# Kernel tuning notes

Hardware: AMD Instinct MI355X
Metric: run time of the kernel (lower is better)

The kernel has to match this reference:

```python
import jax, jax.numpy as jnp
import numpy as np

B, F, S, P, E, H = 64, 32, 512, 96, 8, 2048
TOP_K = 2
ALPHA = 10.0
ENT_EPS = 1e-8
CV_EPS = 1e-10


def setup_inputs() -> dict:
    key = jax.random.key(0)
    ks = jax.random.split(key, 8)
    s = 0.02
    return {
        "x": jax.random.normal(ks[0], (B, F, S), dtype=jnp.float32),
        "time_embedding": jax.random.normal(ks[1], (B, F, S), dtype=jnp.float32),
        "Wg": jax.random.normal(ks[2], (S, E), dtype=jnp.float32) * s,
        "bg": jnp.zeros((E,), dtype=jnp.float32),
        "W1": jax.random.normal(ks[3], (E, S, H), dtype=jnp.float32) * s,
        "b1": jnp.zeros((E, H), dtype=jnp.float32),
        "W2": jax.random.normal(ks[4], (E, H, P), dtype=jnp.float32) * s,
        "b2": jnp.zeros((E, P), dtype=jnp.float32),
    }


def _gates(tf, Wg, bg):
    # tf: [F, B, S] -> logits [F, B, E]
    logits = jnp.einsum('fbs,se->fbe', tf, Wg) + bg
    # kthvalue(x, E - top_k + 1) = (E - top_k)-th entry (0-based) of ascending sort = k-th largest
    kth = jnp.sort(logits, axis=-1)[..., E - TOP_K]  # [F, B]
    mask = logits < kth[..., None]
    sm = jax.nn.softmax(logits, axis=-1)
    dec = jnp.where(mask, ALPHA * jnp.log(sm + 1.0), ALPHA * (jnp.exp(sm) - 1.0))
    return jax.nn.softmax(dec, axis=-1)  # [F, B, E]


def reference(x, time_embedding, Wg, bg, W1, b1, W2, b2):
    xf = jnp.transpose(x, (1, 0, 2))               # [F, B, S]
    tf = jnp.transpose(time_embedding, (1, 0, 2))  # [F, B, S]
    gates = _gates(tf, Wg, bg)                     # [F, B, E]

    # all experts on all features (eval mode: dropout = identity)
    h = jax.nn.gelu(jnp.einsum('fbs,esh->febh', xf, W1) + b1[None, :, None, :], approximate=False)
    eo = jnp.einsum('febh,ehp->febp', h, W2) + b2[None, :, None, :]  # [F, E, B, P]
    out = jnp.einsum('fbe,febp->fbp', gates, eo)   # gated weighted sum
    output = jnp.transpose(out, (1, 0, 2))         # [B, F, P]

    # selector loss: cv_squared of importance = gates.sum(batch) expanded over pred_len
    gsum = gates.sum(axis=1)                       # [F, E]
    imp = jnp.broadcast_to(gsum[..., None], (F, E, P)).reshape(F, E * P)
    cv = jnp.var(imp, axis=1, ddof=1) / (jnp.mean(imp, axis=1) ** 2 + CV_EPS)
    selector_loss = jnp.sum(cv)                    # loss_coef = 1.0

    # entropy loss: importance1 = gates.mean(batch) expanded over pred_len
    gmean = gates.mean(axis=1)                     # [F, E]
    imp1 = jnp.broadcast_to(gmean[..., None], (F, E, P))
    entropy_loss = jnp.sum((-imp1 * jnp.log(imp1 + ENT_EPS)).mean(axis=(1, 2)))

    return output, selector_loss, entropy_loss
```

## Files before the change

### kernel.cpp

```cpp
#include <hip/hip_runtime.h>
#include <math.h>

#define B_ 64
#define F_ 32
#define S_ 512
#define P_ 96
#define E_ 8
#define H_ 2048
#define M_ 2048

#define BM 128
#define BH 128
#define BK 64
#define ZSPLIT 2
#define HPZ (H_ / ZSPLIT)
#define NHT (HPZ / BH)
#define NKC (S_ / BK)

typedef __bf16 bf16x8 __attribute__((ext_vector_type(8)));
typedef __bf16 bf16x4 __attribute__((ext_vector_type(4)));
typedef float f32x4 __attribute__((ext_vector_type(4)));

#define MFMA16(a, b, c) __builtin_amdgcn_mfma_f32_16x16x32_bf16((a), (b), (c), 0, 0, 0)

#define GLL16(gp, lp) __builtin_amdgcn_global_load_lds(                     \
    (const __attribute__((address_space(1))) void*)(gp),                    \
    (__attribute__((address_space(3))) void*)(lp), 16, 0, 0)

#define PW4 asm volatile("s_waitcnt vmcnt(4) lgkmcnt(0)\n\ts_barrier" ::: "memory")
#define PW2 asm volatile("s_waitcnt vmcnt(2) lgkmcnt(0)\n\ts_barrier" ::: "memory")
#define PW0 asm volatile("s_waitcnt vmcnt(0) lgkmcnt(0)\n\ts_barrier" ::: "memory")

__device__ __forceinline__ float fast_gelu(float x) {
  float e = __builtin_amdgcn_exp2f(-2.45546696f * x);
  return x * __builtin_amdgcn_rcpf(1.0f + e);
}

#define PREP_GRID 3776

__global__ __launch_bounds__(256) void k_prep(const float* __restrict__ x,
                                              const float* __restrict__ te,
                                              const float* __restrict__ Wg,
                                              const float* __restrict__ bg,
                                              const float* __restrict__ W1,
                                              const float* __restrict__ W2,
                                              __bf16* __restrict__ xbf,
                                              __bf16* __restrict__ w1t,
                                              __bf16* __restrict__ w2t,
                                              float* __restrict__ gates,
                                              float* __restrict__ out) {
  __shared__ float tile[64 * 65];
  const int blk = blockIdx.x;
  const int tid = threadIdx.x;

  if (blk < 2048) {
    int e = blk >> 8, tt = blk & 255;
    int si = tt >> 5, hi = tt & 31;
    const float* src = W1 + (size_t)e * S_ * H_ + (size_t)(si * 64) * H_ + hi * 64;
    {
      int row = tid >> 2;
      int cb = (tid & 3) * 16;
#pragma unroll
      for (int k = 0; k < 4; ++k) {
        f32x4 v = *(const f32x4*)(src + (size_t)row * H_ + cb + k * 4);
#pragma unroll
        for (int u = 0; u < 4; ++u) tile[row * 65 + cb + k * 4 + u] = v[u];
      }
    }
    __syncthreads();
    {
      int h = tid >> 2;
      int sb = (tid & 3) * 16;
      __bf16* dst = w1t + (size_t)e * H_ * S_ + (size_t)(hi * 64 + h) * S_ + si * 64 + sb;
      bf16x8 o0, o1;
#pragma unroll
      for (int k = 0; k < 8; ++k) o0[k] = (__bf16)tile[(sb + k) * 65 + h];
#pragma unroll
      for (int k = 0; k < 8; ++k) o1[k] = (__bf16)tile[(sb + 8 + k) * 65 + h];
      *(bf16x8*)dst = o0;
      *(bf16x8*)(dst + 8) = o1;
    }
    return;
  }
  if (blk < 2560) {
    int t = blk - 2048;
    int e = t >> 6, hi = (t >> 1) & 31, ph = t & 1;
    const float* src = W2 + (size_t)e * H_ * P_ + (size_t)(hi * 64) * P_ + ph * 48;
    {
      int h = tid & 63;
      int seg = tid >> 6;
#pragma unroll
      for (int k = 0; k < 3; ++k) {
        f32x4 v = *(const f32x4*)(src + (size_t)h * P_ + seg * 12 + k * 4);
#pragma unroll
        for (int u = 0; u < 4; ++u) tile[h * 49 + seg * 12 + k * 4 + u] = v[u];
      }
    }
    __syncthreads();
    if (tid < 192) {
      int p = tid >> 2;
      int hb = (tid & 3) * 16;
      __bf16* dst = w2t + (size_t)e * P_ * H_ + (size_t)(ph * 48 + p) * H_ + hi * 64 + hb;
      bf16x8 o0, o1;
#pragma unroll
      for (int k = 0; k < 8; ++k) o0[k] = (__bf16)tile[(hb + k) * 49 + p];
#pragma unroll
      for (int k = 0; k < 8; ++k) o1[k] = (__bf16)tile[(hb + 8 + k) * 49 + p];
      *(bf16x8*)dst = o0;
      *(bf16x8*)(dst + 8) = o1;
    }
    return;
  }
  if (blk < 3072) {
    size_t i = (size_t)(blk - 2560) * 2048 + (size_t)tid * 8;
#pragma unroll
    for (int k = 0; k < 2; ++k) {
      f32x4 v = *(const f32x4*)(x + i + k * 4);
      bf16x4 o = {(__bf16)v[0], (__bf16)v[1], (__bf16)v[2], (__bf16)v[3]};
      *(bf16x4*)(xbf + i + k * 4) = o;
    }
    return;
  }
  if (blk < 3584) {
    int wave = tid >> 6, lane = tid & 63;
    int m = (blk - 3072) * 4 + wave;
    const float* trow = te + (size_t)m * S_;
    float acc[E_];
#pragma unroll
    for (int e = 0; e < E_; ++e) acc[e] = 0.f;
    for (int s = lane; s < S_; s += 64) {
      float t = trow[s];
      const f32x4* wgr = (const f32x4*)(Wg + s * E_);
      f32x4 a = wgr[0], b = wgr[1];
      acc[0] += t * a[0]; acc[1] += t * a[1]; acc[2] += t * a[2]; acc[3] += t * a[3];
      acc[4] += t * b[0]; acc[5] += t * b[1]; acc[6] += t * b[2]; acc[7] += t * b[3];
    }
#pragma unroll
    for (int e = 0; e < E_; ++e) {
#pragma unroll
      for (int off = 32; off > 0; off >>= 1) acc[e] += __shfl_xor(acc[e], off, 64);
    }
    if (lane == 0) {
      float lg[E_];
      float m1 = -3.4e38f, m2 = -3.4e38f;
#pragma unroll
      for (int e = 0; e < E_; ++e) {
        float v = acc[e] + bg[e];
        lg[e] = v;
        if (v > m1) { m2 = m1; m1 = v; }
        else if (v > m2) { m2 = v; }
      }
      float den = 0.f, sm[E_];
#pragma unroll
      for (int e = 0; e < E_; ++e) { sm[e] = expf(lg[e] - m1); den += sm[e]; }
      float inv = 1.f / den;
      float dmax = -3.4e38f, dec[E_];
#pragma unroll
      for (int e = 0; e < E_; ++e) {
        float p = sm[e] * inv;
        float d = (lg[e] < m2) ? (10.f * logf(p + 1.f)) : (10.f * (expf(p) - 1.f));
        dec[e] = d;
        dmax = fmaxf(dmax, d);
      }
      float dden = 0.f;
#pragma unroll
      for (int e = 0; e < E_; ++e) { dec[e] = expf(dec[e] - dmax); dden += dec[e]; }
      float dinv = 1.f / dden;
#pragma unroll
      for (int e = 0; e < E_; ++e) gates[m * E_ + e] = dec[e] * dinv;
    }
    return;
  }
  {
    size_t i = (size_t)(blk - 3584) * 1024 + (size_t)tid * 4;
    f32x4 z4 = {0.f, 0.f, 0.f, 0.f};
    *(f32x4*)(out + i) = z4;
  }
}

__global__ __launch_bounds__(512, 2) void k_experts(
    const __bf16* __restrict__ xbf,
    const __bf16* __restrict__ w1t,
    const __bf16* __restrict__ w2t,
    const float* __restrict__ b1,
    const float* __restrict__ b2,
    const float* __restrict__ gates,
    float* __restrict__ out)
{
  __shared__ __align__(16) __bf16 W1s[4][BH * BK];
  __shared__ __align__(16) __bf16 Xs[3][BM * BK];
  __shared__ __align__(16) __bf16 Hs[BM * 128];

  const int tid = threadIdx.x;

  if (blockIdx.z == ZSPLIT) {
    if (blockIdx.x != 0 || blockIdx.y != 0) return;
    float* gsum = (float*)&W1s[0][0];
    float* cvs  = gsum + F_ * E_;
    float* ents = cvs + F_;
    if (tid < 256) {
      int f = tid >> 3, ee = tid & 7;
      float s = 0.f;
      for (int b = 0; b < B_; ++b) s += gates[(size_t)(b * F_ + f) * E_ + ee];
      gsum[f * E_ + ee] = s;
    }
    __syncthreads();
    if (tid < F_) {
      float mean = 0.f;
#pragma unroll
      for (int k = 0; k < E_; ++k) mean += gsum[tid * E_ + k];
      mean *= (1.f / E_);
      float ss = 0.f;
#pragma unroll
      for (int k = 0; k < E_; ++k) { float d = gsum[tid * E_ + k] - mean; ss += d * d; }
      float var = (float)P_ * ss / (float)(E_ * P_ - 1);
      cvs[tid] = var / (mean * mean + 1e-10f);
      float ent = 0.f;
#pragma unroll
      for (int k = 0; k < E_; ++k) { float g = gsum[tid * E_ + k] * (1.f / B_); ent += -g * logf(g + 1e-8f); }
      ents[tid] = ent * (1.f / E_);
    }
    __syncthreads();
    if (tid == 0) {
      float a = 0.f, b = 0.f;
      for (int k = 0; k < F_; ++k) { a += cvs[k]; b += ents[k]; }
      out[(size_t)M_ * P_ + 0] = a;
      out[(size_t)M_ * P_ + 1] = b;
    }
    return;
  }

  const int wave = tid >> 6, lane = tid & 63;
  const int l15 = lane & 15, quad = lane >> 4;
  const int e = blockIdx.x;
  const int m0 = blockIdx.y * BM;
  const int hz = blockIdx.z * HPZ;

  const int sg = lane & 7;
  const int srl = lane >> 3;
  const int gcol = ((sg ^ srl) * 8);

  const __bf16* w1base = w1t + ((size_t)e * H_ + hz + wave * 16 + srl) * S_ + gcol;
  const __bf16* xg = xbf + (size_t)(m0 + wave * 16 + srl) * S_ + gcol;
  const __bf16* w2z = w2t + (size_t)e * P_ * H_ + hz;

  const int hq = (wave & 1) * 64;
  const int mq = (wave >> 1) * 32;
  const int w16 = wave * 16;

  const f32x4 fz = {0.f, 0.f, 0.f, 0.f};
  f32x4 acc1[4][2];
  f32x4 acc2[6];
#pragma unroll
  for (int j = 0; j < 6; ++j) acc2[j] = fz;

  auto STAGE_W1 = [&](int slot, const __bf16* src) {
#pragma unroll
    for (int p = 0; p < 2; ++p)
      GLL16(src + (size_t)(p * 8) * S_, &W1s[slot][(wave * 16 + p * 8) * BK]);
  };
  auto STAGE_X = [&](int slot, const __bf16* src) {
#pragma unroll
    for (int p = 0; p < 2; ++p)
      GLL16(src + (size_t)(p * 8) * S_, &Xs[slot][(wave * 16 + p * 8) * BK]);
  };

  auto COMPUTE = [&](const __bf16* w1s, const __bf16* xs) {
#pragma unroll
    for (int kk = 0; kk < 2; ++kk) {
      bf16x8 af[4], bx[2];
#pragma unroll
      for (int i = 0; i < 4; ++i) {
        int r = hq + i * 16 + l15;
        af[i] = *(const bf16x8*)&w1s[r * BK + (((kk * 4 + quad) ^ (r & 7)) * 8)];
      }
#pragma unroll
      for (int j = 0; j < 2; ++j) {
        int r = mq + j * 16 + l15;
        bx[j] = *(const bf16x8*)&xs[r * BK + (((kk * 4 + quad) ^ (r & 7)) * 8)];
      }
      __builtin_amdgcn_s_setprio(1);
#pragma unroll
      for (int i = 0; i < 4; ++i)
#pragma unroll
        for (int j = 0; j < 2; ++j)
          acc1[i][j] = MFMA16(af[i], bx[j], acc1[i][j]);
      __builtin_amdgcn_s_setprio(0);
    }
  };

  auto GEMM2 = [&](int htc) {
    const __bf16* w2c = w2z + htc * BH;
    __builtin_amdgcn_s_setprio(1);
#pragma unroll
    for (int kk = 0; kk < 4; ++kk) {
      int ab = (((w16 + l15) * 256) + (kk * 32 + quad * 8) * 2) ^ ((l15 & 7) << 4);
      bf16x8 a = *(const bf16x8*)((const char*)Hs + ab);
#pragma unroll
      for (int j = 0; j < 6; ++j) {
        bf16x8 bb = *(const bf16x8*)(w2c + (size_t)(j * 16 + l15) * H_ + kk * 32 + quad * 8);
        acc2[j] = MFMA16(a, bb, acc2[j]);
      }
    }
    __builtin_amdgcn_s_setprio(0);
  };

  auto GELU = [&](int ht_) {
    const float* b1w = b1 + (size_t)e * H_ + hz + ht_ * BH + hq;
#pragma unroll
    for (int i = 0; i < 4; ++i) {
      f32x4 bv = *(const f32x4*)(b1w + i * 16 + quad * 4);
#pragma unroll
      for (int j = 0; j < 2; ++j) {
        bf16x4 hv;
#pragma unroll
        for (int r = 0; r < 4; ++r)
          hv[r] = (__bf16)fast_gelu(acc1[i][j][r] + bv[r]);
        int m = mq + j * 16 + l15;
        int wb = (m * 256 + (hq + i * 16 + quad * 4) * 2) ^ ((l15 & 7) << 4);
        *(bf16x4*)((char*)Hs + wb) = hv;
      }
    }
  };

  STAGE_W1(0, w1base);
  STAGE_W1(1, w1base + BK);
  STAGE_X(0, xg);

  int xcur = 0;
  for (int ht = 0; ht < NHT; ++ht) {
#pragma unroll
    for (int i = 0; i < 4; ++i)
#pragma unroll
      for (int j = 0; j < 2; ++j) acc1[i][j] = fz;

    const __bf16* w1h = w1base + (size_t)(ht * BH) * S_;
    const bool tail = (ht == NHT - 1);

#pragma unroll
    for (int kc = 0; kc < NKC; ++kc) {
      if (kc <= 5) {
        STAGE_W1((kc + 2) & 3, w1h + (kc + 2) * BK);
      } else if (!tail) {
        STAGE_W1((kc + 2) & 3, w1h + (size_t)BH * S_ + ((kc + 2) & 7) * BK);
      }
      int xnext = (xcur == 2) ? 0 : xcur + 1;
      if (!(tail && kc == 7)) STAGE_X(xnext, xg + ((kc + 1) & 7) * BK);

      if (!tail || kc <= 5)      { PW4; }
      else if (kc == 6)          { PW2; }
      else                       { PW0; }

      if (kc == 0 && ht > 0) GEMM2(ht - 1);

      COMPUTE(&W1s[kc & 3][0], &Xs[xcur][0]);
      xcur = xnext;
    }
    GELU(ht);
  }
  asm volatile("s_waitcnt lgkmcnt(0)\n\ts_barrier" ::: "memory");
  GEMM2(NHT - 1);

#pragma unroll
  for (int r = 0; r < 4; ++r) {
    int m = m0 + w16 + quad * 4 + r;
    float g = gates[m * E_ + e];
#pragma unroll
    for (int j = 0; j < 6; ++j) {
      int col = j * 16 + l15;
      float v = acc2[j][r];
      if (blockIdx.z == 0) v += b2[e * P_ + col];
      atomicAdd(&out[(size_t)m * P_ + col], g * v);
    }
  }
}

extern "C" void kernel_launch(void* const* d_in, const int* in_sizes, int n_in,
                              void* d_out, int out_size, void* d_ws, size_t ws_size,
                              hipStream_t stream) {
  const float* x  = (const float*)d_in[0];
  const float* te = (const float*)d_in[1];
  const float* Wg = (const float*)d_in[2];
  const float* bg = (const float*)d_in[3];
  const float* W1 = (const float*)d_in[4];
  const float* b1 = (const float*)d_in[5];
  const float* W2 = (const float*)d_in[6];
  const float* b2 = (const float*)d_in[7];
  float* out = (float*)d_out;

  char* ws = (char*)d_ws;
  float* gates = (float*)ws;
  __bf16* xbf  = (__bf16*)(ws + 65536);
  __bf16* w1t  = (__bf16*)(ws + 65536 + 2097152);
  __bf16* w2t  = (__bf16*)(ws + 65536 + 2097152 + 16777216);

  k_prep<<<PREP_GRID, 256, 0, stream>>>(x, te, Wg, bg, W1, W2, xbf, w1t, w2t, gates, out);
  k_experts<<<dim3(E_, M_ / BM, ZSPLIT + 1), 512, 0, stream>>>(xbf, w1t, w2t, b1, b2, gates, out);
}
```

Measured before the change: 205.8 us.

## Load X fragments into registers, shrink LDS buffers, double H split for occupancy

```diff
diff --git a/kernel.cpp b/kernel.cpp
--- a/kernel.cpp
+++ b/kernel.cpp
@@ -12,7 +12,7 @@
 #define BM 128
 #define BH 128
 #define BK 64
-#define ZSPLIT 2
+#define ZSPLIT 4
 #define HPZ (H_ / ZSPLIT)
 #define NHT (HPZ / BH)
 #define NKC (S_ / BK)
@@ -26,10 +26,6 @@
 #define GLL16(gp, lp) __builtin_amdgcn_global_load_lds(                     \
     (const __attribute__((address_space(1))) void*)(gp),                    \
     (__attribute__((address_space(3))) void*)(lp), 16, 0, 0)
-
-#define PW4 asm volatile("s_waitcnt vmcnt(4) lgkmcnt(0)\n\ts_barrier" ::: "memory")
-#define PW2 asm volatile("s_waitcnt vmcnt(2) lgkmcnt(0)\n\ts_barrier" ::: "memory")
-#define PW0 asm volatile("s_waitcnt vmcnt(0) lgkmcnt(0)\n\ts_barrier" ::: "memory")
 
 __device__ __forceinline__ float fast_gelu(float x) {
   float e = __builtin_amdgcn_exp2f(-2.45546696f * x);
@@ -178,7 +174,7 @@
   }
 }
 
-__global__ __launch_bounds__(512, 2) void k_experts(
+__global__ __launch_bounds__(512, 4) void k_experts(
     const __bf16* __restrict__ xbf,
     const __bf16* __restrict__ w1t,
     const __bf16* __restrict__ w2t,
@@ -187,8 +183,7 @@
     const float* __restrict__ gates,
     float* __restrict__ out)
 {
-  __shared__ __align__(16) __bf16 W1s[4][BH * BK];
-  __shared__ __align__(16) __bf16 Xs[3][BM * BK];
+  __shared__ __align__(16) __bf16 W1s[2][BH * BK];
   __shared__ __align__(16) __bf16 Hs[BM * 128];
 
   const int tid = threadIdx.x;
@@ -241,13 +236,15 @@
   const int gcol = ((sg ^ srl) * 8);
 
   const __bf16* w1base = w1t + ((size_t)e * H_ + hz + wave * 16 + srl) * S_ + gcol;
-  const __bf16* xg = xbf + (size_t)(m0 + wave * 16 + srl) * S_ + gcol;
   const __bf16* w2z = w2t + (size_t)e * P_ * H_ + hz;
 
   const int hq = (wave & 1) * 64;
   const int mq = (wave >> 1) * 32;
   const int w16 = wave * 16;
 
+  const __bf16* xr0 = xbf + (size_t)(m0 + mq + l15) * S_ + quad * 8;
+  const __bf16* xr1 = xr0 + (size_t)16 * S_;
+
   const f32x4 fz = {0.f, 0.f, 0.f, 0.f};
   f32x4 acc1[4][2];
   f32x4 acc2[6];
@@ -259,39 +256,31 @@
     for (int p = 0; p < 2; ++p)
       GLL16(src + (size_t)(p * 8) * S_, &W1s[slot][(wave * 16 + p * 8) * BK]);
   };
-  auto STAGE_X = [&](int slot, const __bf16* src) {
-#pragma unroll
-    for (int p = 0; p < 2; ++p)
-      GLL16(src + (size_t)(p * 8) * S_, &Xs[slot][(wave * 16 + p * 8) * BK]);
-  };
-
-  auto COMPUTE = [&](const __bf16* w1s, const __bf16* xs) {
+
+  bf16x8 bc00, bc01, bc10, bc11;
+  bf16x8 bn00, bn01, bn10, bn11;
+
+  auto COMPUTE = [&](const __bf16* w1s) {
 #pragma unroll
     for (int kk = 0; kk < 2; ++kk) {
-      bf16x8 af[4], bx[2];
+      bf16x8 af[4];
 #pragma unroll
       for (int i = 0; i < 4; ++i) {
         int r = hq + i * 16 + l15;
         af[i] = *(const bf16x8*)&w1s[r * BK + (((kk * 4 + quad) ^ (r & 7)) * 8)];
       }
-#pragma unroll
-      for (int j = 0; j < 2; ++j) {
-        int r = mq + j * 16 + l15;
-        bx[j] = *(const bf16x8*)&xs[r * BK + (((kk * 4 + quad) ^ (r & 7)) * 8)];
-      }
-      __builtin_amdgcn_s_setprio(1);
-#pragma unroll
-      for (int i = 0; i < 4; ++i)
-#pragma unroll
-        for (int j = 0; j < 2; ++j)
-          acc1[i][j] = MFMA16(af[i], bx[j], acc1[i][j]);
-      __builtin_amdgcn_s_setprio(0);
+      bf16x8 b0 = kk ? bc01 : bc00;
+      bf16x8 b1f = kk ? bc11 : bc10;
+#pragma unroll
+      for (int i = 0; i < 4; ++i) {
+        acc1[i][0] = MFMA16(af[i], b0, acc1[i][0]);
+        acc1[i][1] = MFMA16(af[i], b1f, acc1[i][1]);
+      }
     }
   };
 
   auto GEMM2 = [&](int htc) {
     const __bf16* w2c = w2z + htc * BH;
-    __builtin_amdgcn_s_setprio(1);
 #pragma unroll
     for (int kk = 0; kk < 4; ++kk) {
       int ab = (((w16 + l15) * 256) + (kk * 32 + quad * 8) * 2) ^ ((l15 & 7) << 4);
@@ -302,7 +291,6 @@
         acc2[j] = MFMA16(a, bb, acc2[j]);
       }
     }
-    __builtin_amdgcn_s_setprio(0);
   };
 
   auto GELU = [&](int ht_) {
@@ -324,10 +312,13 @@
   };
 
   STAGE_W1(0, w1base);
-  STAGE_W1(1, w1base + BK);
-  STAGE_X(0, xg);
-
-  int xcur = 0;
+  bc00 = *(const bf16x8*)(xr0);
+  bc01 = *(const bf16x8*)(xr0 + 32);
+  bc10 = *(const bf16x8*)(xr1);
+  bc11 = *(const bf16x8*)(xr1 + 32);
+  __syncthreads();
+
+#pragma unroll
   for (int ht = 0; ht < NHT; ++ht) {
 #pragma unroll
     for (int i = 0; i < 4; ++i)
@@ -335,30 +326,30 @@
       for (int j = 0; j < 2; ++j) acc1[i][j] = fz;
 
     const __bf16* w1h = w1base + (size_t)(ht * BH) * S_;
-    const bool tail = (ht == NHT - 1);
 
 #pragma unroll
     for (int kc = 0; kc < NKC; ++kc) {
-      if (kc <= 5) {
-        STAGE_W1((kc + 2) & 3, w1h + (kc + 2) * BK);
-      } else if (!tail) {
-        STAGE_W1((kc + 2) & 3, w1h + (size_t)BH * S_ + ((kc + 2) & 7) * BK);
-      }
-      int xnext = (xcur == 2) ? 0 : xcur + 1;
-      if (!(tail && kc == 7)) STAGE_X(xnext, xg + ((kc + 1) & 7) * BK);
-
-      if (!tail || kc <= 5)      { PW4; }
-      else if (kc == 6)          { PW2; }
-      else                       { PW0; }
-
+      if (kc < NKC - 1) {
+        STAGE_W1((kc + 1) & 1, w1h + (kc + 1) * BK);
+      } else if (ht < NHT - 1) {
+        STAGE_W1((kc + 1) & 1, w1h + (size_t)BH * S_);
+      }
+      if (!(ht == NHT - 1 && kc == NKC - 1)) {
+        int kn = ((kc + 1) & 7) * 64;
+        bn00 = *(const bf16x8*)(xr0 + kn);
+        bn01 = *(const bf16x8*)(xr0 + kn + 32);
+        bn10 = *(const bf16x8*)(xr1 + kn);
+        bn11 = *(const bf16x8*)(xr1 + kn + 32);
+      }
       if (kc == 0 && ht > 0) GEMM2(ht - 1);
 
-      COMPUTE(&W1s[kc & 3][0], &Xs[xcur][0]);
-      xcur = xnext;
+      COMPUTE(&W1s[kc & 1][0]);
+      __syncthreads();
+      bc00 = bn00; bc01 = bn01; bc10 = bn10; bc11 = bn11;
     }
     GELU(ht);
-  }
-  asm volatile("s_waitcnt lgkmcnt(0)\n\ts_barrier" ::: "memory");
+    __syncthreads();
+  }
   GEMM2(NHT - 1);
 
 #pragma unroll
```

New measurement: 245.6 us. +19.3%, slower.
